# Optimization experiments

Measured on AMD Instinct MI355X. Metric: run time of the kernel, lower is better.

The kernel has to match this reference:

```python
import jax, jax.numpy as jnp
import numpy as np

N = 100000
E = 1600000
D_IN = 128
D_OUT = 64


def setup_inputs() -> dict:
    key = jax.random.key(0)
    k1, k2, k3, k4, k5 = jax.random.split(key, 5)
    x = jax.random.normal(k1, (N, D_IN), dtype=jnp.float32)
    edge_row = jax.random.randint(k2, (E,), 0, N, dtype=jnp.int32)
    edge_col = jax.random.randint(k3, (E,), 0, N, dtype=jnp.int32)
    edge_val = jax.random.uniform(k4, (E,), dtype=jnp.float32)
    # Glorot-uniform init as in the torch module
    init_range = np.sqrt(6.0 / (D_IN + D_OUT))
    weight = jax.random.uniform(k5, (D_IN, D_OUT), dtype=jnp.float32,
                                minval=-init_range, maxval=init_range)
    return {"x": x, "edge_row": edge_row, "edge_col": edge_col,
            "edge_val": edge_val, "weight": weight}


def reference(x, edge_row, edge_col, edge_val, weight):
    # Dense projection: [N, D_in] @ [D_in, D_out] -> [N, D_out]
    xw = jnp.matmul(x, weight)
    # Sparse aggregation (SpMM with COO support): out[r] += val * xw[c]
    msgs = edge_val[:, None] * xw[edge_col]          # [E, D_out]
    out = jax.ops.segment_sum(msgs, edge_row, num_segments=x.shape[0])
    # bias=False, activation=relu
    return jax.nn.relu(out)
```

## Files before the change

kernel.cpp:

```cpp
#include <hip/hip_runtime.h>

#define NN 100000
#define DIN 128
#define DOUT 64
#define NE 1600000

#define BSHIFT 6
#define BROWS 64
#define NB 1563
#define CAP 1536
#define EPB 8192

#define XWB_B  0u
#define GCUR_B 12800000u
#define BPAD_B (GCUR_B + 8192u)
#define WS_NEED (BPAD_B + (unsigned)NB * CAP * 8u)

typedef unsigned short u16;
typedef unsigned int u32;
typedef __attribute__((ext_vector_type(8))) short v8s;
typedef __attribute__((ext_vector_type(4))) float v4f;

__device__ __forceinline__ float bf2f(u16 u) {
  return __uint_as_float(((u32)u) << 16);
}
__device__ __forceinline__ u16 f2bf(float f) {
  u32 x = __float_as_uint(f);
  u32 r = x + 0x7fffu + ((x >> 16) & 1u);
  return (u16)(r >> 16);
}

__global__ __launch_bounds__(256) void gemm_kernel(
    const float* __restrict__ x, const float* __restrict__ w,
    u16* __restrict__ xwb) {
  __shared__ u16 wlds[16 * 64 * 8];
  const int t = threadIdx.x;
  const int lane = t & 63;
  const int wv = t >> 6;

  #pragma unroll
  for (int pi = 0; pi < 4; ++pi) {
    const int p = t * 4 + pi;
    const int f = p >> 6, lp = p & 63;
    const int kc = f >> 2, nc = f & 3;
    const int kg = lp >> 4, lr = lp & 15;
    const int kbase = kc * 32 + kg * 8;
    u32 pk[4];
    #pragma unroll
    for (int h = 0; h < 4; ++h) {
      const u32 lo = f2bf(w[(kbase + 2 * h)     * DOUT + nc * 16 + lr]);
      const u32 hi = f2bf(w[(kbase + 2 * h + 1) * DOUT + nc * 16 + lr]);
      pk[h] = lo | (hi << 16);
    }
    *reinterpret_cast<uint4*>(&wlds[p * 8]) =
        make_uint4(pk[0], pk[1], pk[2], pk[3]);
  }
  __syncthreads();

  const int row0 = blockIdx.x * 64 + wv * 16;
  if (row0 >= NN) return;
  const int lrow = lane & 15;
  const int lkg  = lane >> 4;

  v8s Bf[4][4];
  #pragma unroll
  for (int kc = 0; kc < 4; ++kc)
    #pragma unroll
    for (int nc = 0; nc < 4; ++nc)
      Bf[kc][nc] = *reinterpret_cast<const v8s*>(
          &wlds[((kc * 4 + nc) * 64 + lane) * 8]);

  const float* xr = x + (size_t)(row0 + lrow) * DIN + lkg * 8;
  float4 xa[4][2];
  #pragma unroll
  for (int kc = 0; kc < 4; ++kc) {
    xa[kc][0] = *reinterpret_cast<const float4*>(xr + kc * 32);
    xa[kc][1] = *reinterpret_cast<const float4*>(xr + kc * 32 + 4);
  }

  v4f acc[4];
  #pragma unroll
  for (int nc = 0; nc < 4; ++nc) acc[nc] = (v4f){0.f, 0.f, 0.f, 0.f};

  #pragma unroll
  for (int kc = 0; kc < 4; ++kc) {
    v8s Af;
    Af[0] = (short)f2bf(xa[kc][0].x);
    Af[1] = (short)f2bf(xa[kc][0].y);
    Af[2] = (short)f2bf(xa[kc][0].z);
    Af[3] = (short)f2bf(xa[kc][0].w);
    Af[4] = (short)f2bf(xa[kc][1].x);
    Af[5] = (short)f2bf(xa[kc][1].y);
    Af[6] = (short)f2bf(xa[kc][1].z);
    Af[7] = (short)f2bf(xa[kc][1].w);
    #pragma unroll
    for (int nc = 0; nc < 4; ++nc)
      acc[nc] = __builtin_amdgcn_mfma_f32_16x16x32_bf16(Af, Bf[kc][nc],
                                                        acc[nc], 0, 0, 0);
  }

  #pragma unroll
  for (int nc = 0; nc < 4; ++nc)
    #pragma unroll
    for (int j = 0; j < 4; ++j)
      xwb[(size_t)(row0 + lkg * 4 + j) * DOUT + nc * 16 + lrow] =
          f2bf(acc[nc][j]);
}

__global__ __launch_bounds__(1024) void place_kernel(
    const int* __restrict__ erow, const int* __restrict__ ecol,
    const float* __restrict__ eval_, int* __restrict__ gcur,
    int2* __restrict__ bpad) {
  __shared__ int hist[NB];
  __shared__ int base[NB];
  __shared__ int lcur[NB];
  const int t = threadIdx.x;
  for (int i = t; i < NB; i += 1024) { hist[i] = 0; lcur[i] = 0; }
  __syncthreads();

  const int e0 = blockIdx.x * EPB;
  const int e1 = min(e0 + EPB, NE);
  for (int e = e0 + t; e < e1; e += 1024)
    atomicAdd(&hist[erow[e] >> BSHIFT], 1);
  __syncthreads();

  for (int i = t; i < NB; i += 1024) {
    const int h = hist[i];
    base[i] = h ? atomicAdd(&gcur[i], h) : 0;
  }
  __syncthreads();

  for (int e = e0 + t; e < e1; e += 1024) {
    const int r = erow[e];
    const int b = r >> BSHIFT;
    const int rank = base[b] + atomicAdd(&lcur[b], 1);
    if (rank < CAP) {
      int2 q;
      q.x = ((r & (BROWS - 1)) << 17) | ecol[e];
      q.y = __float_as_int(eval_[e]);
      bpad[(long)b * CAP + rank] = q;
    }
  }
}

__global__ __launch_bounds__(256) void agg2_kernel(
    const int* __restrict__ gcur, const int2* __restrict__ bpad,
    const u16* __restrict__ xwb, float* __restrict__ out) {
  __shared__ int2 dst[CAP];
  __shared__ int  hist[BROWS];
  __shared__ int  lptr[BROWS + 1];
  __shared__ int  cur[BROWS];

  const int bucket = blockIdx.x;
  const int t = threadIdx.x;
  const int count = min(gcur[bucket], CAP);
  const long sbase = (long)bucket * CAP;

  if (t < BROWS) hist[t] = 0;
  __syncthreads();

  for (int e = t; e < count; e += 256)
    atomicAdd(&hist[(bpad[sbase + e].x >> 17) & (BROWS - 1)], 1);
  __syncthreads();

  if (t < 64) {
    const int v = hist[t];
    int s = v;
    #pragma unroll
    for (int o = 1; o < 64; o <<= 1) {
      const int u = __shfl_up(s, o);
      if (t >= o) s += u;
    }
    lptr[t + 1] = s;
    cur[t] = s - v;
    if (t == 0) lptr[0] = 0;
  }
  __syncthreads();

  for (int e = t; e < count; e += 256) {
    const int2 q = bpad[sbase + e];
    const int r = (q.x >> 17) & (BROWS - 1);
    const int pos = atomicAdd(&cur[r], 1);
    dst[pos] = q;
  }
  __syncthreads();

  const int lane = t & 63;
  const int wave = t >> 6;
  const int row0 = bucket << BSHIFT;
  for (int r = wave; r < BROWS; r += 4) {
    const int row = row0 + r;
    if (row >= NN) break;
    const int s = lptr[r], en = lptr[r + 1];
    float a0 = 0.f, a1 = 0.f, a2 = 0.f, a3 = 0.f;
    float a4 = 0.f, a5 = 0.f, a6 = 0.f, a7 = 0.f;
    int e = s;
    for (; e + 8 <= en; e += 8) {
      const int2 q0 = dst[e],     q1 = dst[e + 1];
      const int2 q2 = dst[e + 2], q3 = dst[e + 3];
      const int2 q4 = dst[e + 4], q5 = dst[e + 5];
      const int2 q6 = dst[e + 6], q7 = dst[e + 7];
      const float g0 = bf2f(xwb[(q0.x & 0x1FFFF) * DOUT + lane]);
      const float g1 = bf2f(xwb[(q1.x & 0x1FFFF) * DOUT + lane]);
      const float g2 = bf2f(xwb[(q2.x & 0x1FFFF) * DOUT + lane]);
      const float g3 = bf2f(xwb[(q3.x & 0x1FFFF) * DOUT + lane]);
      const float g4 = bf2f(xwb[(q4.x & 0x1FFFF) * DOUT + lane]);
      const float g5 = bf2f(xwb[(q5.x & 0x1FFFF) * DOUT + lane]);
      const float g6 = bf2f(xwb[(q6.x & 0x1FFFF) * DOUT + lane]);
      const float g7 = bf2f(xwb[(q7.x & 0x1FFFF) * DOUT + lane]);
      a0 = fmaf(__int_as_float(q0.y), g0, a0);
      a1 = fmaf(__int_as_float(q1.y), g1, a1);
      a2 = fmaf(__int_as_float(q2.y), g2, a2);
      a3 = fmaf(__int_as_float(q3.y), g3, a3);
      a4 = fmaf(__int_as_float(q4.y), g4, a4);
      a5 = fmaf(__int_as_float(q5.y), g5, a5);
      a6 = fmaf(__int_as_float(q6.y), g6, a6);
      a7 = fmaf(__int_as_float(q7.y), g7, a7);
    }
    for (; e + 4 <= en; e += 4) {
      const int2 q0 = dst[e],     q1 = dst[e + 1];
      const int2 q2 = dst[e + 2], q3 = dst[e + 3];
      const float g0 = bf2f(xwb[(q0.x & 0x1FFFF) * DOUT + lane]);
      const float g1 = bf2f(xwb[(q1.x & 0x1FFFF) * DOUT + lane]);
      const float g2 = bf2f(xwb[(q2.x & 0x1FFFF) * DOUT + lane]);
      const float g3 = bf2f(xwb[(q3.x & 0x1FFFF) * DOUT + lane]);
      a0 = fmaf(__int_as_float(q0.y), g0, a0);
      a1 = fmaf(__int_as_float(q1.y), g1, a1);
      a2 = fmaf(__int_as_float(q2.y), g2, a2);
      a3 = fmaf(__int_as_float(q3.y), g3, a3);
    }
    for (; e < en; ++e) {
      const int2 q = dst[e];
      a0 = fmaf(__int_as_float(q.y), bf2f(xwb[(q.x & 0x1FFFF) * DOUT + lane]), a0);
    }
    out[row * DOUT + lane] =
        fmaxf(((a0 + a1) + (a2 + a3)) + ((a4 + a5) + (a6 + a7)), 0.f);
  }
}

__global__ __launch_bounds__(256) void scatter_kernel(
    const int* __restrict__ erow, const int* __restrict__ ecol,
    const float* __restrict__ eval_, const u16* __restrict__ xwb,
    float* __restrict__ out) {
  const int wave = (blockIdx.x * blockDim.x + threadIdx.x) >> 6;
  const int lane = threadIdx.x & 63;
  const int nwaves = (gridDim.x * blockDim.x) >> 6;
  const int per = (NE + nwaves - 1) / nwaves;
  const int e0 = wave * per;
  const int e1 = min(e0 + per, NE);
  for (int base = e0; base < e1; base += 64) {
    const int e = base + lane;
    int r = 0, c = 0; float v = 0.f;
    if (e < e1) { r = erow[e]; c = ecol[e]; v = eval_[e]; }
    const int cnt = min(64, e1 - base);
    for (int j = 0; j < cnt; ++j) {
      const int rj = __shfl(r, j);
      const int cj = __shfl(c, j);
      const float vj = __shfl(v, j);
      atomicAdd(&out[rj * DOUT + lane], vj * bf2f(xwb[cj * DOUT + lane]));
    }
  }
}

__global__ __launch_bounds__(256) void finish_kernel(float* __restrict__ out) {
  const int idx = (blockIdx.x * blockDim.x + threadIdx.x) * 4;
  if (idx < NN * DOUT) {
    float4 a = *reinterpret_cast<const float4*>(&out[idx]);
    a.x = fmaxf(a.x, 0.f); a.y = fmaxf(a.y, 0.f);
    a.z = fmaxf(a.z, 0.f); a.w = fmaxf(a.w, 0.f);
    *reinterpret_cast<float4*>(&out[idx]) = a;
  }
}

extern "C" void kernel_launch(void* const* d_in, const int* in_sizes, int n_in,
                              void* d_out, int out_size, void* d_ws, size_t ws_size,
                              hipStream_t stream) {
  const float* x     = (const float*)d_in[0];
  const int*   erow  = (const int*)d_in[1];
  const int*   ecol  = (const int*)d_in[2];
  const float* eval_ = (const float*)d_in[3];
  const float* w     = (const float*)d_in[4];
  float* out = (float*)d_out;

  char* ws = (char*)d_ws;
  u16* xwb = (u16*)(ws + XWB_B);

  const int gemm_grid = (NN + 63) / 64;
  gemm_kernel<<<gemm_grid, 256, 0, stream>>>(x, w, xwb);

  if (ws_size >= (size_t)WS_NEED) {
    int*  gcur = (int*)(ws + GCUR_B);
    int2* bpad = (int2*)(ws + BPAD_B);

    hipMemsetAsync(gcur, 0, NB * 4, stream);
    const int place_grid = (NE + EPB - 1) / EPB;
    place_kernel<<<place_grid, 1024, 0, stream>>>(erow, ecol, eval_, gcur, bpad);
    agg2_kernel<<<NB, 256, 0, stream>>>(gcur, bpad, xwb, out);
  } else {
    hipMemsetAsync(d_out, 0, (size_t)NN * DOUT * sizeof(float), stream);
    scatter_kernel<<<2048, 256, 0, stream>>>(erow, ecol, eval_, xwb, out);
    const int fin_grid = (NN * DOUT / 4 + 255) / 256;
    finish_kernel<<<fin_grid, 256, 0, stream>>>(out);
  }
}
```

Before: 86.37 us.

## Cache bucket entries in registers and gather four edges per wave with vector loads

The bucket's edge records are loaded once into registers and reused for both the histogram and the scatter-to-LDS passes, rather than reading global memory twice. The aggregation loop is reorganized so each wave processes four edges at once: 16 lanes per edge each load 4 bf16 values (8 bytes), and the partial sums are then combined with cross-lane shuffles and written as float4. The aim is to cut the number of gather instructions and raise memory-level parallelism. The cost is extra shuffle reductions, padded iterations for short rows, and a hardcoded six-entry register cache that assumes CAP/256 entries per thread.

```diff
diff --git a/kernel.cpp b/kernel.cpp
--- a/kernel.cpp
+++ b/kernel.cpp
@@ -159,8 +159,15 @@
   if (t < BROWS) hist[t] = 0;
   __syncthreads();
 
-  for (int e = t; e < count; e += 256)
-    atomicAdd(&hist[(bpad[sbase + e].x >> 17) & (BROWS - 1)], 1);
+  int2 qr[6];
+  #pragma unroll
+  for (int k = 0; k < 6; ++k) {
+    const int e = t + k * 256;
+    if (e < count) {
+      qr[k] = bpad[sbase + e];
+      atomicAdd(&hist[(qr[k].x >> 17) & (BROWS - 1)], 1);
+    }
+  }
   __syncthreads();
 
   if (t < 64) {
@@ -177,64 +184,65 @@
   }
   __syncthreads();
 
-  for (int e = t; e < count; e += 256) {
-    const int2 q = bpad[sbase + e];
-    const int r = (q.x >> 17) & (BROWS - 1);
-    const int pos = atomicAdd(&cur[r], 1);
-    dst[pos] = q;
+  #pragma unroll
+  for (int k = 0; k < 6; ++k) {
+    const int e = t + k * 256;
+    if (e < count) {
+      const int r = (qr[k].x >> 17) & (BROWS - 1);
+      const int pos = atomicAdd(&cur[r], 1);
+      dst[pos] = qr[k];
+    }
   }
   __syncthreads();
 
   const int lane = t & 63;
   const int wave = t >> 6;
+  const int slot = lane >> 4;
+  const int li   = lane & 15;
   const int row0 = bucket << BSHIFT;
+  const int cmax = count - 1;
+
   for (int r = wave; r < BROWS; r += 4) {
     const int row = row0 + r;
     if (row >= NN) break;
     const int s = lptr[r], en = lptr[r + 1];
     float a0 = 0.f, a1 = 0.f, a2 = 0.f, a3 = 0.f;
-    float a4 = 0.f, a5 = 0.f, a6 = 0.f, a7 = 0.f;
-    int e = s;
-    for (; e + 8 <= en; e += 8) {
-      const int2 q0 = dst[e],     q1 = dst[e + 1];
-      const int2 q2 = dst[e + 2], q3 = dst[e + 3];
-      const int2 q4 = dst[e + 4], q5 = dst[e + 5];
-      const int2 q6 = dst[e + 6], q7 = dst[e + 7];
-      const float g0 = bf2f(xwb[(q0.x & 0x1FFFF) * DOUT + lane]);
-      const float g1 = bf2f(xwb[(q1.x & 0x1FFFF) * DOUT + lane]);
-      const float g2 = bf2f(xwb[(q2.x & 0x1FFFF) * DOUT + lane]);
-      const float g3 = bf2f(xwb[(q3.x & 0x1FFFF) * DOUT + lane]);
-      const float g4 = bf2f(xwb[(q4.x & 0x1FFFF) * DOUT + lane]);
-      const float g5 = bf2f(xwb[(q5.x & 0x1FFFF) * DOUT + lane]);
-      const float g6 = bf2f(xwb[(q6.x & 0x1FFFF) * DOUT + lane]);
-      const float g7 = bf2f(xwb[(q7.x & 0x1FFFF) * DOUT + lane]);
-      a0 = fmaf(__int_as_float(q0.y), g0, a0);
-      a1 = fmaf(__int_as_float(q1.y), g1, a1);
-      a2 = fmaf(__int_as_float(q2.y), g2, a2);
-      a3 = fmaf(__int_as_float(q3.y), g3, a3);
-      a4 = fmaf(__int_as_float(q4.y), g4, a4);
-      a5 = fmaf(__int_as_float(q5.y), g5, a5);
-      a6 = fmaf(__int_as_float(q6.y), g6, a6);
-      a7 = fmaf(__int_as_float(q7.y), g7, a7);
-    }
-    for (; e + 4 <= en; e += 4) {
-      const int2 q0 = dst[e],     q1 = dst[e + 1];
-      const int2 q2 = dst[e + 2], q3 = dst[e + 3];
-      const float g0 = bf2f(xwb[(q0.x & 0x1FFFF) * DOUT + lane]);
-      const float g1 = bf2f(xwb[(q1.x & 0x1FFFF) * DOUT + lane]);
-      const float g2 = bf2f(xwb[(q2.x & 0x1FFFF) * DOUT + lane]);
-      const float g3 = bf2f(xwb[(q3.x & 0x1FFFF) * DOUT + lane]);
-      a0 = fmaf(__int_as_float(q0.y), g0, a0);
-      a1 = fmaf(__int_as_float(q1.y), g1, a1);
-      a2 = fmaf(__int_as_float(q2.y), g2, a2);
-      a3 = fmaf(__int_as_float(q3.y), g3, a3);
-    }
-    for (; e < en; ++e) {
-      const int2 q = dst[e];
-      a0 = fmaf(__int_as_float(q.y), bf2f(xwb[(q.x & 0x1FFFF) * DOUT + lane]), a0);
-    }
-    out[row * DOUT + lane] =
-        fmaxf(((a0 + a1) + (a2 + a3)) + ((a4 + a5) + (a6 + a7)), 0.f);
+    for (int e = s; e < en; e += 8) {
+      {
+        const int idx = e + slot;
+        const int2 q = dst[min(idx, cmax)];
+        const float v = (idx < en) ? __int_as_float(q.y) : 0.f;
+        const u32 col = (u32)q.x & 0x1FFFFu;
+        const uint2 g = *reinterpret_cast<const uint2*>(
+            xwb + (size_t)col * DOUT + li * 4);
+        a0 = fmaf(v, __uint_as_float(g.x << 16), a0);
+        a1 = fmaf(v, __uint_as_float(g.x & 0xFFFF0000u), a1);
+        a2 = fmaf(v, __uint_as_float(g.y << 16), a2);
+        a3 = fmaf(v, __uint_as_float(g.y & 0xFFFF0000u), a3);
+      }
+      {
+        const int idx = e + 4 + slot;
+        const int2 q = dst[min(idx, cmax)];
+        const float v = (idx < en) ? __int_as_float(q.y) : 0.f;
+        const u32 col = (u32)q.x & 0x1FFFFu;
+        const uint2 g = *reinterpret_cast<const uint2*>(
+            xwb + (size_t)col * DOUT + li * 4);
+        a0 = fmaf(v, __uint_as_float(g.x << 16), a0);
+        a1 = fmaf(v, __uint_as_float(g.x & 0xFFFF0000u), a1);
+        a2 = fmaf(v, __uint_as_float(g.y << 16), a2);
+        a3 = fmaf(v, __uint_as_float(g.y & 0xFFFF0000u), a3);
+      }
+    }
+    a0 += __shfl_xor(a0, 16); a0 += __shfl_xor(a0, 32);
+    a1 += __shfl_xor(a1, 16); a1 += __shfl_xor(a1, 32);
+    a2 += __shfl_xor(a2, 16); a2 += __shfl_xor(a2, 32);
+    a3 += __shfl_xor(a3, 16); a3 += __shfl_xor(a3, 32);
+    if (slot == 0) {
+      float4 o;
+      o.x = fmaxf(a0, 0.f); o.y = fmaxf(a1, 0.f);
+      o.z = fmaxf(a2, 0.f); o.w = fmaxf(a3, 0.f);
+      *reinterpret_cast<float4*>(&out[(size_t)row * DOUT + li * 4]) = o;
+    }
   }
 }
 
```

Result: faster. 79.71 us (-7.7%).
